# Kernel tuning notes

Hardware: AMD Instinct MI355X
Metric: run time of the kernel (lower is better)

## Reference

```python
import jax, jax.numpy as jnp
import numpy as np

D, B, N, DIM, H, DH, MLP = 6, 4, 1024, 768, 12, 64, 3072
SCALE = DH ** -0.5
EPS = 1e-5


def setup_inputs() -> dict:
    key = jax.random.key(0)
    ks = jax.random.split(key, 5)
    s = 0.02
    return {
        "x": jax.random.normal(ks[0], (B, N, DIM), jnp.float32),
        "ln1_g": jnp.ones((D, DIM), jnp.float32),
        "ln1_b": jnp.zeros((D, DIM), jnp.float32),
        "wqkv": jax.random.normal(ks[1], (D, DIM, 3 * H * DH), jnp.float32) * s,
        "wo": jax.random.normal(ks[2], (D, H * DH, DIM), jnp.float32) * s,
        "bo": jnp.zeros((D, DIM), jnp.float32),
        "ln2_g": jnp.ones((D, DIM), jnp.float32),
        "ln2_b": jnp.zeros((D, DIM), jnp.float32),
        "w1": jax.random.normal(ks[3], (D, DIM, MLP), jnp.float32) * s,
        "b1": jnp.zeros((D, MLP), jnp.float32),
        "w2": jax.random.normal(ks[4], (D, MLP, DIM), jnp.float32) * s,
        "b2": jnp.zeros((D, DIM), jnp.float32),
    }


def _ln(h, g, b):
    m = h.mean(-1, keepdims=True)
    v = h.var(-1, keepdims=True)  # biased, matches torch LayerNorm
    return (h - m) / jnp.sqrt(v + EPS) * g + b


def _heads(t):
    # [b, n, h*d] -> [b, h, n, d]
    return t.reshape(B, N, H, DH).transpose(0, 2, 1, 3)


def reference(x, ln1_g, ln1_b, wqkv, wo, bo, ln2_g, ln2_b, w1, b1, w2, b2):
    def step(carry, p):
        xc, _, _ = carry
        g1, be1, Wqkv, Wo, Bo, g2, be2, W1, B1, W2, B2 = p
        h = _ln(xc, g1, be1)
        q, k, v = jnp.split(h @ Wqkv, 3, axis=-1)
        q, k, v = _heads(q), _heads(k), _heads(v)
        attn = jax.nn.softmax(jnp.einsum('bhid,bhjd->bhij', q, k) * SCALE, axis=-1)
        out = jnp.einsum('bhij,bhjd->bhid', attn, v)
        out = out.transpose(0, 2, 1, 3).reshape(B, N, H * DH)
        xc = xc + out @ Wo + Bo
        h2 = _ln(xc, g2, be2)
        xc = xc + jax.nn.gelu(h2 @ W1 + B1, approximate=False) @ W2 + B2
        return (xc, k, v), None

    kv0 = jnp.zeros((B, H, N, DH), x.dtype)
    (xf, k, v), _ = jax.lax.scan(
        step, (x, kv0, kv0),
        (ln1_g, ln1_b, wqkv, wo, bo, ln2_g, ln2_b, w1, b1, w2, b2))
    return xf, k, v
```

## Files before the change

### kernel.cpp

```cpp
#include <hip/hip_runtime.h>
#include <hip/hip_bf16.h>
#include <math.h>

typedef __bf16 bf16;
typedef __bf16 bf16x8 __attribute__((ext_vector_type(8)));
typedef float f32x4 __attribute__((ext_vector_type(4)));

enum { EPI_QKV = 0, EPI_GELU = 1 };

__device__ __forceinline__ void gload16(const void* g, void* s) {
  __builtin_amdgcn_global_load_lds((__attribute__((address_space(1))) void*)g,
                                   (__attribute__((address_space(3))) void*)s, 16, 0, 0);
}

#define MFMA16(a, b, c) __builtin_amdgcn_mfma_f32_16x16x32_bf16((a), (b), (c), 0, 0, 0)

__device__ __forceinline__ void xcd_swizzle(int& bx, int& by) {
  const int gx = gridDim.x, nwg = gx * gridDim.y;
  int bid = blockIdx.y * gx + blockIdx.x;
  if ((nwg & 7) == 0) bid = (bid & 7) * (nwg >> 3) + (bid >> 3);
  bx = bid % gx;
  by = bid / gx;
}

__global__ __launch_bounds__(256) void cast_x(const float* __restrict__ x,
                                              float* __restrict__ xq) {
  const int i = (blockIdx.x * 256 + threadIdx.x) * 4;
  float4 v = *(const float4*)(x + i);
  v.x = (float)(bf16)v.x; v.y = (float)(bf16)v.y;
  v.z = (float)(bf16)v.z; v.w = (float)(bf16)v.w;
  *(float4*)(xq + i) = v;
}

__global__ __launch_bounds__(256) void wconv_all(
    const float* __restrict__ wqkv, const float* __restrict__ wo,
    const float* __restrict__ w1, const float* __restrict__ w2,
    bf16* __restrict__ qkvT, bf16* __restrict__ woT,
    bf16* __restrict__ w1T, bf16* __restrict__ w2T, int lfix) {
  __shared__ float tile[32][33];
  const int bid = blockIdx.x;
  int l, r;
  if (lfix < 0) { l = bid / 6912; r = bid % 6912; } else { l = lfix; r = bid; }
  const int lo = (lfix < 0) ? l : 0;
  const float* W; bf16* Wt; int K, N, tt;
  if (r < 1728)      { W = wqkv + (size_t)l * 768 * 2304; Wt = qkvT + (size_t)lo * 2304 * 768; K = 768;  N = 2304; tt = r; }
  else if (r < 2304) { W = wo   + (size_t)l * 768 * 768;  Wt = woT  + (size_t)lo * 768 * 768;  K = 768;  N = 768;  tt = r - 1728; }
  else if (r < 4608) { W = w1   + (size_t)l * 768 * 3072; Wt = w1T  + (size_t)lo * 3072 * 768; K = 768;  N = 3072; tt = r - 2304; }
  else               { W = w2   + (size_t)l * 3072 * 768; Wt = w2T  + (size_t)lo * 768 * 3072; K = 3072; N = 768;  tt = r - 4608; }
  const int ntx = N >> 5;
  const int n0 = (tt % ntx) * 32, k0 = (tt / ntx) * 32;
  const int tx = threadIdx.x & 31, ty = threadIdx.x >> 5;
#pragma unroll
  for (int rr = 0; rr < 4; ++rr)
    tile[ty + rr * 8][tx] = W[(size_t)(k0 + ty + rr * 8) * N + n0 + tx];
  __syncthreads();
#pragma unroll
  for (int rr = 0; rr < 4; ++rr)
    Wt[(size_t)(n0 + ty + rr * 8) * K + k0 + tx] = (bf16)tile[tx][ty + rr * 8];
}

__global__ __launch_bounds__(256) void ln_kernel(const float* __restrict__ x,
                                                 const float* __restrict__ g,
                                                 const float* __restrict__ b,
                                                 bf16* __restrict__ out) {
  const int row = blockIdx.x, t = threadIdx.x;
  const float* xr = x + (size_t)row * 768;
  float v0 = xr[t], v1 = xr[t + 256], v2 = xr[t + 512];
  float s = v0 + v1 + v2, sq = v0 * v0 + v1 * v1 + v2 * v2;
#pragma unroll
  for (int m = 32; m; m >>= 1) { s += __shfl_xor(s, m); sq += __shfl_xor(sq, m); }
  __shared__ float rs[4], rq[4];
  const int w = t >> 6;
  if ((t & 63) == 0) { rs[w] = s; rq[w] = sq; }
  __syncthreads();
  s = rs[0] + rs[1] + rs[2] + rs[3];
  sq = rq[0] + rq[1] + rq[2] + rq[3];
  const float mean = s * (1.f / 768.f);
  const float var = sq * (1.f / 768.f) - mean * mean;
  const float rstd = rsqrtf(var + 1e-5f);
  bf16* orow = out + (size_t)row * 768;
  orow[t]       = (bf16)((v0 - mean) * rstd * g[t]       + b[t]);
  orow[t + 256] = (bf16)((v1 - mean) * rstd * g[t + 256] + b[t + 256]);
  orow[t + 512] = (bf16)((v2 - mean) * rstd * g[t + 512] + b[t + 512]);
}

template <int EPI>
__global__ __launch_bounds__(256) void gemm_s(
    const bf16* __restrict__ A, const bf16* __restrict__ Bt,
    const float* __restrict__ bias, bf16* __restrict__ Cb,
    bf16* __restrict__ qo, bf16* __restrict__ ko_, bf16* __restrict__ vo,
    float* __restrict__ kf, float* __restrict__ vf, int wf,
    int M, int Nc, int K) {
  __shared__ __align__(16) char lds[2][2][8192];
  const int t = threadIdx.x, lane = t & 63, w = t >> 6;
  const int wr = w >> 1, wc = w & 1;
  int bx, by;
  xcd_swizzle(bx, by);
  const size_t m0 = (size_t)by * 128, n0 = (size_t)bx * 128;

  const char* ab[2]; const char* bb[2];
#pragma unroll
  for (int r = 0; r < 2; ++r) {
    int c = r * 256 + t;
    ab[r] = (const char*)(A + (m0 + (c >> 2)) * (size_t)K) + (c & 3) * 16;
    bb[r] = (const char*)(Bt + (n0 + (c >> 2)) * (size_t)K) + (c & 3) * 16;
  }

  f32x4 acc[4][4] = {};

  auto stage = [&](int buf, int tt) {
#pragma unroll
    for (int r = 0; r < 2; ++r) {
      gload16(ab[r] + (size_t)tt * 64, &lds[buf][0][r * 4096 + w * 1024]);
      gload16(bb[r] + (size_t)tt * 64, &lds[buf][1][r * 4096 + w * 1024]);
    }
  };
  auto compute = [&](int buf) {
    const char* As = lds[buf][0];
    const char* Bs = lds[buf][1];
    const int ko = (lane >> 4) * 16;
    bf16x8 af[4], fb[4];
#pragma unroll
    for (int i = 0; i < 4; ++i) {
      af[i] = *(const bf16x8*)(As + (wr * 64 + i * 16 + (lane & 15)) * 64 + ko);
      fb[i] = *(const bf16x8*)(Bs + (wc * 64 + i * 16 + (lane & 15)) * 64 + ko);
    }
#pragma unroll
    for (int mi = 0; mi < 4; ++mi)
#pragma unroll
      for (int ni = 0; ni < 4; ++ni)
        acc[mi][ni] = MFMA16(af[mi], fb[ni], acc[mi][ni]);
  };

  const int NT = K >> 5;
  stage(0, 0);
  __syncthreads();
  int cur = 0;
  for (int tt = 1; tt < NT; ++tt) {
    stage(cur ^ 1, tt);
    compute(cur);
    __syncthreads();
    cur ^= 1;
  }
  compute(cur);

#pragma unroll
  for (int mi = 0; mi < 4; ++mi) {
#pragma unroll
    for (int i = 0; i < 4; ++i) {
      size_t row = m0 + wr * 64 + mi * 16 + ((lane >> 4) << 2) + i;
#pragma unroll
      for (int ni = 0; ni < 4; ++ni) {
        size_t col = n0 + wc * 64 + ni * 16 + (lane & 15);
        float v = acc[mi][ni][i];
        if (EPI == EPI_GELU) {
          v += bias[col];
          v = 0.5f * v * (1.f + erff(v * 0.70710678118f));
          Cb[row * (size_t)Nc + col] = (bf16)v;
        } else {
          int b = (int)(row >> 10), n = (int)(row & 1023);
          int which = (int)col >= 1536 ? 2 : ((int)col >= 768 ? 1 : 0);
          int hd = (int)col - which * 768;
          int hh = hd >> 6, d = hd & 63;
          size_t dst = ((size_t)(b * 12 + hh) * 1024 + n) * 64 + d;
          if (which == 0) {
            qo[dst] = (bf16)v;
          } else if (which == 1) {
            ko_[dst] = (bf16)v;
            if (wf) kf[dst] = v;
          } else {
            vo[dst] = (bf16)v;
            if (wf) vf[dst] = v;
          }
        }
      }
    }
  }
}

__global__ __launch_bounds__(256) void gemm64_s(
    const bf16* __restrict__ A, const bf16* __restrict__ Bt,
    const float* __restrict__ bias, const float* __restrict__ res,
    float* __restrict__ Cf, int M, int Nc, int K) {
  __shared__ __align__(16) char lds[2][12288];
  const int t = threadIdx.x, lane = t & 63, w = t >> 6;
  const int wr = w >> 1, wc = w & 1;
  const int l15 = lane & 15, l4 = lane >> 4;
  int bx, by;
  xcd_swizzle(bx, by);
  const size_t m0 = (size_t)by * 64, n0 = (size_t)bx * 128;

  const char* ab = (const char*)(A + (m0 + (t >> 2)) * (size_t)K) + (t & 3) * 16;
  const char* b0 = (const char*)(Bt + (n0 + (t >> 2)) * (size_t)K) + (t & 3) * 16;
  const char* b1 = (const char*)(Bt + (n0 + 64 + (t >> 2)) * (size_t)K) + (t & 3) * 16;

  f32x4 acc[2][4] = {};

  auto stage = [&](int buf, int tt) {
    gload16(ab + (size_t)tt * 64, &lds[buf][t * 16]);
    gload16(b0 + (size_t)tt * 64, &lds[buf][4096 + t * 16]);
    gload16(b1 + (size_t)tt * 64, &lds[buf][8192 + t * 16]);
  };
  auto compute = [&](int buf) {
    const char* L = lds[buf];
    const int ko = l4 * 16;
    bf16x8 fa[2], fb[4];
#pragma unroll
    for (int mi = 0; mi < 2; ++mi)
      fa[mi] = *(const bf16x8*)(L + (wr * 32 + mi * 16 + l15) * 64 + ko);
#pragma unroll
    for (int ni = 0; ni < 4; ++ni)
      fb[ni] = *(const bf16x8*)(L + 4096 + (wc * 64 + ni * 16 + l15) * 64 + ko);
#pragma unroll
    for (int mi = 0; mi < 2; ++mi)
#pragma unroll
      for (int ni = 0; ni < 4; ++ni)
        acc[mi][ni] = MFMA16(fa[mi], fb[ni], acc[mi][ni]);
  };

  const int NT = K >> 5;
  stage(0, 0);
  __syncthreads();
  int cur = 0;
  for (int tt = 1; tt < NT; ++tt) {
    stage(cur ^ 1, tt);
    compute(cur);
    __syncthreads();
    cur ^= 1;
  }
  compute(cur);

#pragma unroll
  for (int mi = 0; mi < 2; ++mi) {
#pragma unroll
    for (int i = 0; i < 4; ++i) {
      size_t row = m0 + wr * 32 + mi * 16 + l4 * 4 + i;
#pragma unroll
      for (int ni = 0; ni < 4; ++ni) {
        size_t col = n0 + wc * 64 + ni * 16 + l15;
        float v = acc[mi][ni][i] + bias[col] + res[row * (size_t)Nc + col];
        Cf[row * (size_t)Nc + col] = v;
      }
    }
  }
}

__global__ __launch_bounds__(256) void vtrans(const bf16* __restrict__ v,
                                              bf16* __restrict__ vT) {
  __shared__ bf16 tile[32][33];
  const int tx = threadIdx.x, ty = threadIdx.y;
  const int bh = blockIdx.x, n0 = blockIdx.y * 32, d0 = blockIdx.z * 32;
  const bf16* vb = v + (size_t)bh * 1024 * 64;
  bf16* vTb = vT + (size_t)bh * 64 * 1024;
#pragma unroll
  for (int r = 0; r < 4; ++r)
    tile[ty + r * 8][tx] = vb[(size_t)(n0 + ty + r * 8) * 64 + d0 + tx];
  __syncthreads();
#pragma unroll
  for (int r = 0; r < 4; ++r)
    vTb[(size_t)(d0 + ty + r * 8) * 1024 + n0 + tx] = tile[tx][ty + r * 8];
}

__global__ __launch_bounds__(64) void attn_kernel(const bf16* __restrict__ q,
                                                  const bf16* __restrict__ k,
                                                  const bf16* __restrict__ vT,
                                                  bf16* __restrict__ out) {
  __shared__ __align__(16) char Ps[8192];
  const int bh = blockIdx.x, qb = blockIdx.y;
  const int lane = threadIdx.x & 63;
  const int l15 = lane & 15, l4 = lane >> 4;

  const char* kp = (const char*)(k + (size_t)bh * 1024 * 64);
  const char* vp = (const char*)(vT + (size_t)bh * 64 * 1024);

  bf16x8 aq[2][2];
  {
    const bf16* qbase = q + ((size_t)bh * 1024 + qb * 32) * 64;
#pragma unroll
    for (int mi = 0; mi < 2; ++mi)
#pragma unroll
      for (int ks = 0; ks < 2; ++ks)
        aq[mi][ks] = *(const bf16x8*)(qbase + (mi * 16 + l15) * 64 + ks * 32 + l4 * 8);
  }

  f32x4 oacc[2][4] = {};
  float mrun[2][4], lrun[2][4];
#pragma unroll
  for (int mi = 0; mi < 2; ++mi)
#pragma unroll
    for (int i = 0; i < 4; ++i) { mrun[mi][i] = -1e30f; lrun[mi][i] = 0.f; }

  for (int kb = 0; kb < 8; ++kb) {
    f32x4 sacc[2][8] = {};
#pragma unroll
    for (int ks = 0; ks < 2; ++ks) {
#pragma unroll
      for (int ni = 0; ni < 8; ++ni) {
        const bf16x8 bk = *(const bf16x8*)(kp + (size_t)kb * 16384 +
                                           (ni * 16 + l15) * 128 + ks * 64 + l4 * 16);
        sacc[0][ni] = MFMA16(aq[0][ks], bk, sacc[0][ni]);
        sacc[1][ni] = MFMA16(aq[1][ks], bk, sacc[1][ni]);
      }
    }
#pragma unroll
    for (int mi = 0; mi < 2; ++mi)
#pragma unroll
      for (int ni = 0; ni < 8; ++ni)
        sacc[mi][ni] *= 0.125f;

#pragma unroll
    for (int mi = 0; mi < 2; ++mi) {
#pragma unroll
      for (int i = 0; i < 4; ++i) {
        float mx = sacc[mi][0][i];
#pragma unroll
        for (int ni = 1; ni < 8; ++ni) mx = fmaxf(mx, sacc[mi][ni][i]);
#pragma unroll
        for (int sh = 8; sh; sh >>= 1) mx = fmaxf(mx, __shfl_xor(mx, sh));
        float mnew = fmaxf(mrun[mi][i], mx);
        float alpha = __expf(mrun[mi][i] - mnew);
        mrun[mi][i] = mnew;
        float rsum = 0.f;
#pragma unroll
        for (int ni = 0; ni < 8; ++ni) {
          float pe = __expf(sacc[mi][ni][i] - mnew);
          sacc[mi][ni][i] = pe;
          rsum += pe;
        }
#pragma unroll
        for (int sh = 8; sh; sh >>= 1) rsum += __shfl_xor(rsum, sh);
        lrun[mi][i] = lrun[mi][i] * alpha + rsum;
#pragma unroll
        for (int ni = 0; ni < 4; ++ni) oacc[mi][ni][i] *= alpha;
      }
    }

#pragma unroll
    for (int mi = 0; mi < 2; ++mi)
#pragma unroll
      for (int i = 0; i < 4; ++i) {
        int rowl = mi * 16 + l4 * 4 + i;
        char* prp = Ps + rowl * 256;
        int sw = rowl & 7;
#pragma unroll
        for (int ni = 0; ni < 8; ++ni) {
          int col = ni * 16 + l15;
          *(bf16*)(prp + (((col >> 3) ^ sw) * 16) + (col & 7) * 2) = (bf16)sacc[mi][ni][i];
        }
      }

    const int prow0 = l15, prow1 = 16 + l15;
#pragma unroll
    for (int ks = 0; ks < 4; ++ks) {
      const bf16x8 ap0 = *(const bf16x8*)(Ps + prow0 * 256 + (((ks * 4 + l4) ^ (prow0 & 7)) * 16));
      const bf16x8 ap1 = *(const bf16x8*)(Ps + prow1 * 256 + (((ks * 4 + l4) ^ (prow1 & 7)) * 16));
#pragma unroll
      for (int ni = 0; ni < 4; ++ni) {
        const bf16x8 bv = *(const bf16x8*)(vp + (ni * 16 + l15) * 2048 +
                                           kb * 256 + ks * 64 + l4 * 16);
        oacc[0][ni] = MFMA16(ap0, bv, oacc[0][ni]);
        oacc[1][ni] = MFMA16(ap1, bv, oacc[1][ni]);
      }
    }
  }

  const int b = bh / 12, hh = bh % 12;
#pragma unroll
  for (int mi = 0; mi < 2; ++mi)
#pragma unroll
    for (int i = 0; i < 4; ++i) {
      int n = qb * 32 + mi * 16 + l4 * 4 + i;
      float inv = 1.f / lrun[mi][i];
      bf16* orow = out + ((size_t)b * 1024 + n) * 768 + hh * 64;
#pragma unroll
      for (int ni = 0; ni < 4; ++ni)
        orow[ni * 16 + l15] = (bf16)(oacc[mi][ni][i] * inv);
    }
}

extern "C" void kernel_launch(void* const* d_in, const int* in_sizes, int n_in,
                              void* d_out, int out_size, void* d_ws, size_t ws_size,
                              hipStream_t stream) {
  (void)in_sizes; (void)n_in; (void)out_size;
  const float* x_in = (const float*)d_in[0];
  const float* ln1g = (const float*)d_in[1];
  const float* ln1b = (const float*)d_in[2];
  const float* wqkv = (const float*)d_in[3];
  const float* wo   = (const float*)d_in[4];
  const float* bo   = (const float*)d_in[5];
  const float* ln2g = (const float*)d_in[6];
  const float* ln2b = (const float*)d_in[7];
  const float* w1   = (const float*)d_in[8];
  const float* b1   = (const float*)d_in[9];
  const float* w2   = (const float*)d_in[10];
  const float* b2   = (const float*)d_in[11];

  float* outx = (float*)d_out;
  float* outk = outx + (size_t)4096 * 768;
  float* outv = outk + (size_t)4096 * 768;

  char* p = (char*)d_ws;
  auto take = [&](size_t bytes) {
    char* r = p;
    p += (bytes + 255) & ~(size_t)255;
    return r;
  };
  float* xw   = (float*)take((size_t)4096 * 768 * 4);
  bf16*  h    = (bf16*)take((size_t)4096 * 768 * 2);
  bf16*  mbuf = (bf16*)take((size_t)4096 * 3072 * 2);
  bf16*  qbuf = (bf16*)take((size_t)4096 * 768 * 2);
  bf16*  kbuf = (bf16*)take((size_t)4096 * 768 * 2);
  bf16*  vbuf = (bf16*)take((size_t)4096 * 768 * 2);
  bf16*  vTb  = (bf16*)take((size_t)4096 * 768 * 2);
  bf16*  abuf = (bf16*)take((size_t)4096 * 768 * 2);

  const size_t wq1 = (size_t)2304 * 768, wo1 = (size_t)768 * 768,
               w11 = (size_t)3072 * 768, w21 = (size_t)768 * 3072;
  const size_t used = (size_t)(p - (char*)d_ws);
  const size_t wbytes = (wq1 + wo1 + w11 + w21) * 2;
  const bool hoist = ws_size >= used + 6 * wbytes + 8192;
  const int nl = hoist ? 6 : 1;
  bf16* qkvT = (bf16*)take(wq1 * 2 * nl);
  bf16* woT  = (bf16*)take(wo1 * 2 * nl);
  bf16* w1T  = (bf16*)take(w11 * 2 * nl);
  bf16* w2T  = (bf16*)take(w21 * 2 * nl);

  cast_x<<<3072, 256, 0, stream>>>(x_in, xw);
  if (hoist)
    wconv_all<<<41472, 256, 0, stream>>>(wqkv, wo, w1, w2, qkvT, woT, w1T, w2T, -1);

  for (int l = 0; l < 6; ++l) {
    if (!hoist)
      wconv_all<<<6912, 256, 0, stream>>>(wqkv, wo, w1, w2, qkvT, woT, w1T, w2T, l);
    bf16* qkL = qkvT + (hoist ? (size_t)l * wq1 : 0);
    bf16* woL = woT  + (hoist ? (size_t)l * wo1 : 0);
    bf16* w1L = w1T  + (hoist ? (size_t)l * w11 : 0);
    bf16* w2L = w2T  + (hoist ? (size_t)l * w21 : 0);

    ln_kernel<<<4096, 256, 0, stream>>>(xw, ln1g + l * 768, ln1b + l * 768, h);
    gemm_s<EPI_QKV><<<dim3(18, 32), 256, 0, stream>>>(
        h, qkL, nullptr, nullptr, qbuf, kbuf, vbuf, outk, outv, l == 5 ? 1 : 0,
        4096, 2304, 768);
    vtrans<<<dim3(48, 32, 2), dim3(32, 8), 0, stream>>>(vbuf, vTb);
    attn_kernel<<<dim3(48, 32), 64, 0, stream>>>(qbuf, kbuf, vTb, abuf);
    gemm64_s<<<dim3(6, 64), 256, 0, stream>>>(
        abuf, woL, bo + l * 768, xw, xw, 4096, 768, 768);
    ln_kernel<<<4096, 256, 0, stream>>>(xw, ln2g + l * 768, ln2b + l * 768, h);
    gemm_s<EPI_GELU><<<dim3(24, 32), 256, 0, stream>>>(
        h, w1L, b1 + l * 3072, mbuf, nullptr, nullptr, nullptr, nullptr, nullptr, 0,
        4096, 3072, 768);
    gemm64_s<<<dim3(6, 64), 256, 0, stream>>>(
        mbuf, w2L, b2 + l * 768, xw, xw, 4096, 768, 3072);
  }
  hipMemcpyAsync(d_out, xw, (size_t)4096 * 768 * 4, hipMemcpyDeviceToDevice, stream);
}
```

Baseline: 1.346 ms.

## Split attention key loop across four waves and merge partials in LDS

The attention kernel now launches 256 threads per block. Each of the four waves processes a quarter of the key blocks with its own online-softmax state, and the partial outputs, maxima and sums are then combined through shared memory with a rescaled reduction. The output is written as vectorized bf16x8 stores. The final layer's MLP GEMM writes straight to the output buffer, removing the trailing device-to-device copy. This adds LDS usage and two barriers per block in exchange for shorter per-block serial work.

```diff
diff --git a/kernel.cpp b/kernel.cpp
--- a/kernel.cpp
+++ b/kernel.cpp
@@ -261,13 +261,13 @@
     vTb[(size_t)(d0 + ty + r * 8) * 1024 + n0 + tx] = tile[tx][ty + r * 8];
 }
 
-__global__ __launch_bounds__(64) void attn_kernel(const bf16* __restrict__ q,
-                                                  const bf16* __restrict__ k,
-                                                  const bf16* __restrict__ vT,
-                                                  bf16* __restrict__ out) {
-  __shared__ __align__(16) char Ps[8192];
+__global__ __launch_bounds__(256) void attn_kernel(const bf16* __restrict__ q,
+                                                   const bf16* __restrict__ k,
+                                                   const bf16* __restrict__ vT,
+                                                   bf16* __restrict__ out) {
+  __shared__ __align__(16) char sm[36352];
   const int bh = blockIdx.x, qb = blockIdx.y;
-  const int lane = threadIdx.x & 63;
+  const int t = threadIdx.x, lane = t & 63, w = t >> 6;
   const int l15 = lane & 15, l4 = lane >> 4;
 
   const char* kp = (const char*)(k + (size_t)bh * 1024 * 64);
@@ -290,7 +290,10 @@
 #pragma unroll
     for (int i = 0; i < 4; ++i) { mrun[mi][i] = -1e30f; lrun[mi][i] = 0.f; }
 
-  for (int kb = 0; kb < 8; ++kb) {
+  char* Pw = sm + w * 8192;
+
+  for (int kk = 0; kk < 2; ++kk) {
+    const int kb = w * 2 + kk;
     f32x4 sacc[2][8] = {};
 #pragma unroll
     for (int ks = 0; ks < 2; ++ks) {
@@ -340,7 +343,7 @@
 #pragma unroll
       for (int i = 0; i < 4; ++i) {
         int rowl = mi * 16 + l4 * 4 + i;
-        char* prp = Ps + rowl * 256;
+        char* prp = Pw + rowl * 256;
         int sw = rowl & 7;
 #pragma unroll
         for (int ni = 0; ni < 8; ++ni) {
@@ -352,8 +355,8 @@
     const int prow0 = l15, prow1 = 16 + l15;
 #pragma unroll
     for (int ks = 0; ks < 4; ++ks) {
-      const bf16x8 ap0 = *(const bf16x8*)(Ps + prow0 * 256 + (((ks * 4 + l4) ^ (prow0 & 7)) * 16));
-      const bf16x8 ap1 = *(const bf16x8*)(Ps + prow1 * 256 + (((ks * 4 + l4) ^ (prow1 & 7)) * 16));
+      const bf16x8 ap0 = *(const bf16x8*)(Pw + prow0 * 256 + (((ks * 4 + l4) ^ (prow0 & 7)) * 16));
+      const bf16x8 ap1 = *(const bf16x8*)(Pw + prow1 * 256 + (((ks * 4 + l4) ^ (prow1 & 7)) * 16));
 #pragma unroll
       for (int ni = 0; ni < 4; ++ni) {
         const bf16x8 bv = *(const bf16x8*)(vp + (ni * 16 + l15) * 2048 +
@@ -364,18 +367,49 @@
     }
   }
 
-  const int b = bh / 12, hh = bh % 12;
+  __syncthreads();
+  float* Of = (float*)sm;
+  float* Ml = (float*)(sm + 34816);
+  float* Ll = (float*)(sm + 34816 + 512);
 #pragma unroll
   for (int mi = 0; mi < 2; ++mi)
 #pragma unroll
     for (int i = 0; i < 4; ++i) {
-      int n = qb * 32 + mi * 16 + l4 * 4 + i;
-      float inv = 1.f / lrun[mi][i];
-      bf16* orow = out + ((size_t)b * 1024 + n) * 768 + hh * 64;
+      int row = mi * 16 + l4 * 4 + i;
+      if (l15 == 0) {
+        Ml[w * 32 + row] = mrun[mi][i];
+        Ll[w * 32 + row] = lrun[mi][i];
+      }
 #pragma unroll
       for (int ni = 0; ni < 4; ++ni)
-        orow[ni * 16 + l15] = (bf16)(oacc[mi][ni][i] * inv);
-    }
+        Of[(w * 32 + row) * 68 + ni * 16 + l15] = oacc[mi][ni][i];
+    }
+  __syncthreads();
+
+  {
+    const int rowg = w * 8 + (lane >> 3);
+    const int d0 = (lane & 7) * 8;
+    float M = Ml[rowg];
+#pragma unroll
+    for (int p = 1; p < 4; ++p) M = fmaxf(M, Ml[p * 32 + rowg]);
+    float L = 0.f;
+    float o[8] = {};
+#pragma unroll
+    for (int p = 0; p < 4; ++p) {
+      const float sc = __expf(Ml[p * 32 + rowg] - M);
+      L += Ll[p * 32 + rowg] * sc;
+      const float* op = Of + (p * 32 + rowg) * 68 + d0;
+#pragma unroll
+      for (int j = 0; j < 8; ++j) o[j] += op[j] * sc;
+    }
+    const float inv = 1.f / L;
+    const int b = bh / 12, hh = bh % 12;
+    const int n = qb * 32 + rowg;
+    bf16x8 ov;
+#pragma unroll
+    for (int j = 0; j < 8; ++j) ov[j] = (bf16)(o[j] * inv);
+    *(bf16x8*)(out + ((size_t)b * 1024 + n) * 768 + hh * 64 + d0) = ov;
+  }
 }
 
 extern "C" void kernel_launch(void* const* d_in, const int* in_sizes, int n_in,
@@ -442,7 +476,7 @@
         h, qkL, nullptr, nullptr, qbuf, kbuf, vbuf, outk, outv, l == 5 ? 1 : 0,
         4096, 2304, 768);
     vtrans<<<dim3(48, 32, 2), dim3(32, 8), 0, stream>>>(vbuf, vTb);
-    attn_kernel<<<dim3(48, 32), 64, 0, stream>>>(qbuf, kbuf, vTb, abuf);
+    attn_kernel<<<dim3(48, 32), 256, 0, stream>>>(qbuf, kbuf, vTb, abuf);
     gemm64_s<<<dim3(6, 64), 256, 0, stream>>>(
         abuf, woL, bo + l * 768, xw, xw, 4096, 768, 768);
     ln_kernel<<<4096, 256, 0, stream>>>(xw, ln2g + l * 768, ln2b + l * 768, h);
@@ -450,7 +484,6 @@
         h, w1L, b1 + l * 3072, mbuf, nullptr, nullptr, nullptr, nullptr, nullptr, 0,
         4096, 3072, 768);
     gemm64_s<<<dim3(6, 64), 256, 0, stream>>>(
-        mbuf, w2L, b2 + l * 768, xw, xw, 4096, 768, 3072);
-  }
-  hipMemcpyAsync(d_out, xw, (size_t)4096 * 768 * 4, hipMemcpyDeviceToDevice, stream);
-}
+        mbuf, w2L, b2 + l * 768, xw, (l == 5) ? outx : xw, 4096, 768, 3072);
+  }
+}
```

After: 1.467 ms. 1.09x slower.
